# Optimization experiments

Measured on AMD Instinct MI355X. Metric: run time of the kernel, lower is better.

The kernel has to match this reference:

```python
import jax, jax.numpy as jnp
import numpy as np
import math

N_HEAD = 16
HEAD = 64
WINDOW = 256


def _split_heads(h, B, T):
    # [B,T,C] -> [B,H,T,hs]
    return h.reshape(B, T, N_HEAD, HEAD).transpose(0, 2, 1, 3)


def setup_inputs() -> dict:
    key = jax.random.key(0)
    ks = jax.random.split(key, 16)
    B, T, C = 4, 1024, 1024
    scale = 0.02
    inp = {}
    inp['x'] = jax.random.normal(ks[0], (B, T, C), jnp.float32)
    inp['pos_emb'] = jax.random.normal(ks[1], (B, T, C), jnp.float32)
    for i, n in enumerate(['Wq', 'Wk', 'Wv', 'Wpq', 'Wpk', 'Wo']):
        inp[n] = jax.random.normal(ks[2 + i], (C, C), jnp.float32) * scale
        inp['b' + n[1:]] = jnp.zeros((C,), jnp.float32)
    return inp


def reference(x, pos_emb, Wq, bq, Wk, bk, Wv, bv, Wpq, bpq, Wpk, bpk, Wo, bo):
    B, T, C = x.shape
    q = _split_heads(x @ Wq + bq, B, T)
    k = _split_heads(x @ Wk + bk, B, T)
    v = _split_heads(x @ Wv + bv, B, T)
    pq = _split_heads(pos_emb @ Wpq + bpq, B, T)
    pk = _split_heads(pos_emb @ Wpk + bpk, B, T)

    # content-content scores, pre-scaled by 1/sqrt(hs) as in the original
    wei = jnp.einsum('bhqd,bhkd->bhqk', q, k) * (HEAD ** -0.5)
    # disentangled content->position and position->content terms
    c2p = jnp.einsum('bhqd,bhkd->bhqk', q, pk)
    p2c = jnp.einsum('bhqd,bhkd->bhqk', pq, k)
    wei = (wei + c2p + p2c) * (1.0 / math.sqrt(3 * HEAD))

    # causal + local-window band mask: j <= i and j >= i - WINDOW
    i = jnp.arange(T)
    allowed = (i[None, :] <= i[:, None]) & (i[None, :] >= i[:, None] - WINDOW)
    wei = jnp.where(allowed[None, None], wei, -jnp.inf)

    # ALiBi bias on |i-j| with per-head slopes 2^(-(8/H)*(h+1))
    slopes = 2.0 ** (-(8.0 / N_HEAD) * jnp.arange(1, N_HEAD + 1, dtype=jnp.float32))
    dist = jnp.abs(i[None, :] - i[:, None]).astype(wei.dtype)
    wei = wei - slopes[None, :, None, None] * dist[None, None]

    wei = jax.nn.softmax(wei, axis=-1)  # masked entries -> 0
    out = jnp.einsum('bhqk,bhkd->bhqd', wei, v)
    out = out.transpose(0, 2, 1, 3).reshape(B, T, C)
    return out @ Wo + bo, wei
```

## Files before the change

### kernel.cpp

```cpp
#include <hip/hip_runtime.h>

#define NHEAD 16
#define WIN 256

typedef unsigned short u16;
typedef unsigned int u32;
typedef short bf16x8 __attribute__((ext_vector_type(8)));
typedef float floatx4 __attribute__((ext_vector_type(4)));
typedef u16 u16x4 __attribute__((ext_vector_type(4)));

__device__ __forceinline__ u16 f2bf(float f) {
    u32 u = __builtin_bit_cast(u32, f);
    u32 r = (u + 0x7fffu + ((u >> 16) & 1u)) >> 16;
    return (u16)r;
}
__device__ __forceinline__ float bf2f(u16 b) {
    u32 u = ((u32)b) << 16;
    return __builtin_bit_cast(float, u);
}

__device__ __forceinline__ void gload_lds16(const void* g, void* l) {
    __builtin_amdgcn_global_load_lds((const __attribute__((address_space(1))) u32*)g,
                                     (__attribute__((address_space(3))) u32*)l, 16, 0, 0);
}

__global__ void k_prep_in(const float* __restrict__ x, const float* __restrict__ pos,
                          u16* __restrict__ xb, u16* __restrict__ pb) {
    int i = blockIdx.x * 256 + threadIdx.x;
    const float* src = x; u16* dst = xb;
    int j = i;
    if (i >= 1048576) { src = pos; dst = pb; j = i - 1048576; }
    const floatx4 v = ((const floatx4*)src)[j];
    u16x4 o;
    o[0] = f2bf(v[0]); o[1] = f2bf(v[1]); o[2] = f2bf(v[2]); o[3] = f2bf(v[3]);
    ((u16x4*)dst)[j] = o;
}

__global__ void k_prep_w(const float* __restrict__ Wq, const float* __restrict__ Wk,
                         const float* __restrict__ Wv, const float* __restrict__ Wpq,
                         const float* __restrict__ Wpk, const float* __restrict__ Wo,
                         u16* __restrict__ wtqkv, u16* __restrict__ wtp, u16* __restrict__ wto) {
    __shared__ float tile[32][33];
    const int z = blockIdx.z;
    const float* W; u16* Wt;
    switch (z) {
        case 0: W = Wq;  Wt = wtqkv;           break;
        case 1: W = Wk;  Wt = wtqkv + 1048576; break;
        case 2: W = Wv;  Wt = wtqkv + 2097152; break;
        case 3: W = Wpq; Wt = wtp;             break;
        case 4: W = Wpk; Wt = wtp + 1048576;   break;
        default: W = Wo; Wt = wto;             break;
    }
    const int tx = threadIdx.x & 31, ty = threadIdx.x >> 5;
    const int nb = blockIdx.x << 5, kb = blockIdx.y << 5;
#pragma unroll
    for (int i = 0; i < 4; ++i)
        tile[ty + 8 * i][tx] = W[(size_t)(kb + ty + 8 * i) * 1024 + nb + tx];
    __syncthreads();
#pragma unroll
    for (int i = 0; i < 4; ++i)
        Wt[(size_t)(nb + ty + 8 * i) * 1024 + kb + tx] = f2bf(tile[tx][ty + 8 * i]);
}

__global__ void k_concat_bias(const float* __restrict__ bq, const float* __restrict__ bk,
                              const float* __restrict__ bv, const float* __restrict__ bpq,
                              const float* __restrict__ bpk,
                              float* __restrict__ bqkv, float* __restrict__ bp) {
    int i = blockIdx.x * 256 + threadIdx.x;
    if (i >= 5120) return;
    float v; float* d;
    if (i < 1024)      { v = bq[i];         d = bqkv + i; }
    else if (i < 2048) { v = bk[i - 1024];  d = bqkv + i; }
    else if (i < 3072) { v = bv[i - 2048];  d = bqkv + i; }
    else if (i < 4096) { v = bpq[i - 3072]; d = bp + (i - 3072); }
    else               { v = bpk[i - 4096]; d = bp + (i - 3072); }
    *d = v;
}

__launch_bounds__(256, 2)
__global__ void gemm_proj(const u16* __restrict__ A0, const u16* __restrict__ Bt0,
                          u16* __restrict__ C0, const float* __restrict__ bias0, int nblk0, int N0,
                          const u16* __restrict__ A1, const u16* __restrict__ Bt1,
                          u16* __restrict__ C1, const float* __restrict__ bias1, int N1,
                          int M, int K) {
    __shared__ u16 smA[128 * 64];
    __shared__ u16 smB[128 * 64];
    const int t = threadIdx.x;
    const int l = t & 63, w = t >> 6;
    const int bx = blockIdx.x;
    const u16* A; const u16* Bt; u16* C; const float* bias; int N, n0;
    if (bx < nblk0) { A = A0; Bt = Bt0; C = C0; bias = bias0; N = N0; n0 = bx << 7; }
    else            { A = A1; Bt = Bt1; C = C1; bias = bias1; N = N1; n0 = (bx - nblk0) << 7; }
    const int m0 = blockIdx.y << 7;
    const int wm = w & 1, wn = w >> 1;
    floatx4 acc[4][4];
#pragma unroll
    for (int a = 0; a < 4; ++a)
#pragma unroll
        for (int bq = 0; bq < 4; ++bq) { floatx4 z = {0.f, 0.f, 0.f, 0.f}; acc[a][bq] = z; }

    const int nkt = K >> 6;
    for (int kt = 0; kt < nkt; ++kt) {
        const int k0 = kt << 6;
#pragma unroll
        for (int i = 0; i < 4; ++i) {
            int o = (w << 12) + (i << 10) + (l << 4);
            int row = o >> 7, colb = o & 127;
            int sc = colb ^ ((row & 7) << 4);
            gload_lds16((const char*)A + ((size_t)(m0 + row) * K + k0) * 2 + sc,
                        (char*)smA + (w << 12) + (i << 10));
            gload_lds16((const char*)Bt + ((size_t)(n0 + row) * K + k0) * 2 + sc,
                        (char*)smB + (w << 12) + (i << 10));
        }
        __syncthreads();
#pragma unroll
        for (int ks = 0; ks < 2; ++ks) {
            const int kb = ((ks << 5) + ((l >> 4) << 3)) << 1;
            bf16x8 am[4], bn[4];
#pragma unroll
            for (int mt = 0; mt < 4; ++mt) {
                int row = (wm << 6) + (mt << 4) + (l & 15);
                am[mt] = *(const bf16x8*)((const char*)smA + row * 128 + (kb ^ ((row & 7) << 4)));
            }
#pragma unroll
            for (int nt = 0; nt < 4; ++nt) {
                int row = (wn << 6) + (nt << 4) + (l & 15);
                bn[nt] = *(const bf16x8*)((const char*)smB + row * 128 + (kb ^ ((row & 7) << 4)));
            }
#pragma unroll
            for (int mt = 0; mt < 4; ++mt)
#pragma unroll
                for (int nt = 0; nt < 4; ++nt)
                    acc[mt][nt] = __builtin_amdgcn_mfma_f32_16x16x32_bf16(am[mt], bn[nt], acc[mt][nt], 0, 0, 0);
        }
        __syncthreads();
    }
#pragma unroll
    for (int nt = 0; nt < 4; ++nt) {
        const int n = n0 + (wn << 6) + (nt << 4) + (l & 15);
        const float bv = bias[n];
#pragma unroll
        for (int mt = 0; mt < 4; ++mt) {
#pragma unroll
            for (int r = 0; r < 4; ++r) {
                int m = m0 + (wm << 6) + (mt << 4) + ((l >> 4) << 2) + r;
                C[(size_t)m * N + n] = f2bf(acc[mt][nt][r] + bv);
            }
        }
    }
}

__launch_bounds__(256, 2)
__global__ void gemm_bt_f32(const u16* __restrict__ A, const u16* __restrict__ Bt,
                            float* __restrict__ Cout, const float* __restrict__ bias,
                            int M, int N, int K) {
    __shared__ u16 smA[128 * 64];
    __shared__ u16 smB[128 * 64];
    const int t = threadIdx.x;
    const int l = t & 63, w = t >> 6;
    const int n0 = blockIdx.x << 7, m0 = blockIdx.y << 7;
    const int wm = w & 1, wn = w >> 1;
    floatx4 acc[4][4];
#pragma unroll
    for (int a = 0; a < 4; ++a)
#pragma unroll
        for (int bq = 0; bq < 4; ++bq) { floatx4 z = {0.f, 0.f, 0.f, 0.f}; acc[a][bq] = z; }

    const int nkt = K >> 6;
    for (int kt = 0; kt < nkt; ++kt) {
        const int k0 = kt << 6;
#pragma unroll
        for (int i = 0; i < 4; ++i) {
            int o = (w << 12) + (i << 10) + (l << 4);
            int row = o >> 7, colb = o & 127;
            int sc = colb ^ ((row & 7) << 4);
            gload_lds16((const char*)A + ((size_t)(m0 + row) * K + k0) * 2 + sc,
                        (char*)smA + (w << 12) + (i << 10));
            gload_lds16((const char*)Bt + ((size_t)(n0 + row) * K + k0) * 2 + sc,
                        (char*)smB + (w << 12) + (i << 10));
        }
        __syncthreads();
#pragma unroll
        for (int ks = 0; ks < 2; ++ks) {
            const int kb = ((ks << 5) + ((l >> 4) << 3)) << 1;
            bf16x8 am[4], bn[4];
#pragma unroll
            for (int mt = 0; mt < 4; ++mt) {
                int row = (wm << 6) + (mt << 4) + (l & 15);
                am[mt] = *(const bf16x8*)((const char*)smA + row * 128 + (kb ^ ((row & 7) << 4)));
            }
#pragma unroll
            for (int nt = 0; nt < 4; ++nt) {
                int row = (wn << 6) + (nt << 4) + (l & 15);
                bn[nt] = *(const bf16x8*)((const char*)smB + row * 128 + (kb ^ ((row & 7) << 4)));
            }
#pragma unroll
            for (int mt = 0; mt < 4; ++mt)
#pragma unroll
                for (int nt = 0; nt < 4; ++nt)
                    acc[mt][nt] = __builtin_amdgcn_mfma_f32_16x16x32_bf16(am[mt], bn[nt], acc[mt][nt], 0, 0, 0);
        }
        __syncthreads();
    }
#pragma unroll
    for (int nt = 0; nt < 4; ++nt) {
        const int n = n0 + (wn << 6) + (nt << 4) + (l & 15);
        const float bv = bias[n];
#pragma unroll
        for (int mt = 0; mt < 4; ++mt) {
#pragma unroll
            for (int r = 0; r < 4; ++r) {
                int m = m0 + (wm << 6) + (mt << 4) + ((l >> 4) << 2) + r;
                Cout[(size_t)m * N + n] = acc[mt][nt][r] + bv;
            }
        }
    }
}

__launch_bounds__(256, 2)
__global__ void k_attn(const u16* __restrict__ qkv, const u16* __restrict__ pqk,
                       float* __restrict__ wei, u16* __restrict__ att) {
    __shared__ __align__(16) char sm[50176];
    u16* smQ  = (u16*)(sm);
    u16* smPQ = (u16*)(sm + 8192);
    u16* smK  = (u16*)(sm + 16384);
    u16* smKm = (u16*)(sm + 24576);
    u16* smP  = (u16*)(sm);
    u16* smVt = (u16*)(sm + 41984);

    const int t = threadIdx.x, l = t & 63, w = t >> 6;
    const int qt = blockIdx.x, h = blockIdx.y, b = blockIdx.z;
    const int q0 = qt << 6;
    const int jlo = (q0 - WIN) > 0 ? (q0 - WIN) : 0;
    const int nch = (qt + 1) < 5 ? (qt + 1) : 5;
    const int col_l = l & 15;
    const int rq_hi = (l >> 4) << 2;

#pragma unroll
    for (int i = 0; i < 2; ++i) {
        int o = (w << 11) + (i << 10) + (l << 4);
        int row = o >> 7, colb = o & 127;
        int sc = colb ^ ((row & 7) << 4);
        gload_lds16((const char*)qkv + ((size_t)(b * 1024 + q0 + row) * 3072 + h * 64) * 2 + sc,
                    (char*)smQ + (w << 11) + (i << 10));
        gload_lds16((const char*)pqk + ((size_t)(b * 1024 + q0 + row) * 2048 + h * 64) * 2 + sc,
                    (char*)smPQ + (w << 11) + (i << 10));
    }

    {
        const int zlen1 = jlo;
        const int zstart2 = q0 + 64;
        const int nz4 = (zlen1 + (1024 - zstart2)) >> 2;
        float* wbase = wei + (((size_t)(b * NHEAD + h)) << 20);
        floatx4 z4 = {0.f, 0.f, 0.f, 0.f};
        for (int rr = w; rr < 64; rr += 4) {
            float* rowp = wbase + (((size_t)(q0 + rr)) << 10);
            for (int cc = l; cc < nz4; cc += 64) {
                int off4 = cc << 2;
                int col = (off4 < zlen1) ? off4 : (zstart2 + (off4 - zlen1));
                *(floatx4*)(rowp + col) = z4;
            }
        }
    }

    floatx4 acc[20];
#pragma unroll
    for (int i = 0; i < 20; ++i) { floatx4 z = {0.f, 0.f, 0.f, 0.f}; acc[i] = z; }

    const int prow = t >> 2, pd0 = (t & 3) << 4;
    bf16x8 rk0, rk1, rp0, rp1;
    {
        const u16* kp = qkv + (size_t)(b * 1024 + jlo + prow) * 3072 + 1024 + h * 64 + pd0;
        const u16* pp = pqk + (size_t)(b * 1024 + jlo + prow) * 2048 + 1024 + h * 64 + pd0;
        rk0 = *(const bf16x8*)kp; rk1 = *(const bf16x8*)(kp + 8);
        rp0 = *(const bf16x8*)pp; rp1 = *(const bf16x8*)(pp + 8);
    }
#pragma unroll
    for (int c = 0; c < 5; ++c) {
        if (c < nch) {
            const int jb = jlo + (c << 6);
            {
                bf16x8 o0, o1;
#pragma unroll
                for (int j = 0; j < 8; ++j) {
                    o0[j] = (short)f2bf(0.125f * bf2f((u16)rk0[j]) + bf2f((u16)rp0[j]));
                    o1[j] = (short)f2bf(0.125f * bf2f((u16)rk1[j]) + bf2f((u16)rp1[j]));
                }
                const int sw = (prow & 7) << 4;
                *(bf16x8*)((char*)smKm + prow * 128 + ((pd0 * 2) ^ sw)) = o0;
                *(bf16x8*)((char*)smKm + prow * 128 + ((pd0 * 2 + 16) ^ sw)) = o1;
            }
#pragma unroll
            for (int i = 0; i < 2; ++i) {
                int o = (w << 11) + (i << 10) + (l << 4);
                int row = o >> 7, colb = o & 127;
                int sc = colb ^ ((row & 7) << 4);
                gload_lds16((const char*)qkv + ((size_t)(b * 1024 + jb + row) * 3072 + 1024 + h * 64) * 2 + sc,
                            (char*)smK + (w << 11) + (i << 10));
            }
            __syncthreads();
            if (c + 1 < nch) {
                const int jb2 = jlo + ((c + 1) << 6);
                const u16* kp = qkv + (size_t)(b * 1024 + jb2 + prow) * 3072 + 1024 + h * 64 + pd0;
                const u16* pp = pqk + (size_t)(b * 1024 + jb2 + prow) * 2048 + 1024 + h * 64 + pd0;
                rk0 = *(const bf16x8*)kp; rk1 = *(const bf16x8*)(kp + 8);
                rp0 = *(const bf16x8*)pp; rp1 = *(const bf16x8*)(pp + 8);
            }
            __builtin_amdgcn_s_setprio(1);
#pragma unroll
            for (int ks = 0; ks < 2; ++ks) {
                const int kb = ((ks << 5) + ((l >> 4) << 3)) << 1;
                const int rq = (w << 4) + (l & 15);
                bf16x8 aQ  = *(const bf16x8*)((const char*)smQ  + rq * 128 + (kb ^ ((rq & 7) << 4)));
                bf16x8 aPQ = *(const bf16x8*)((const char*)smPQ + rq * 128 + (kb ^ ((rq & 7) << 4)));
#pragma unroll
                for (int s = 0; s < 4; ++s) {
                    const int rk = (s << 4) + (l & 15);
                    bf16x8 bKm = *(const bf16x8*)((const char*)smKm + rk * 128 + (kb ^ ((rk & 7) << 4)));
                    bf16x8 bK  = *(const bf16x8*)((const char*)smK  + rk * 128 + (kb ^ ((rk & 7) << 4)));
                    acc[c * 4 + s] = __builtin_amdgcn_mfma_f32_16x16x32_bf16(aQ,  bKm, acc[c * 4 + s], 0, 0, 0);
                    acc[c * 4 + s] = __builtin_amdgcn_mfma_f32_16x16x32_bf16(aPQ, bK,  acc[c * 4 + s], 0, 0, 0);
                }
            }
            __builtin_amdgcn_s_setprio(0);
            __syncthreads();
        }
    }

    const float inv_s192 = 0.07216878364870323f;
    const float slope = exp2f(-0.5f * (float)(h + 1));
    const int ntiles = nch << 2;
#pragma unroll
    for (int r = 0; r < 4; ++r) {
        const int iq = q0 + (w << 4) + rq_hi + r;
        float mx = -1e30f;
#pragma unroll
        for (int ti = 0; ti < 20; ++ti) {
            int j = jlo + (ti << 4) + col_l;
            float s = acc[ti][r] * inv_s192 - slope * (float)(iq - j);
            bool ok = (ti < ntiles) && (j <= iq) && (j >= iq - WIN);
            s = ok ? s : -1e30f;
            acc[ti][r] = s;
            mx = fmaxf(mx, s);
        }
        mx = fmaxf(mx, __shfl_xor(mx, 1));
        mx = fmaxf(mx, __shfl_xor(mx, 2));
        mx = fmaxf(mx, __shfl_xor(mx, 4));
        mx = fmaxf(mx, __shfl_xor(mx, 8));
        float sum = 0.f;
#pragma unroll
        for (int ti = 0; ti < 20; ++ti) {
            float p = __expf(acc[ti][r] - mx);
            acc[ti][r] = p;
            sum += p;
        }
        sum += __shfl_xor(sum, 1); sum += __shfl_xor(sum, 2);
        sum += __shfl_xor(sum, 4); sum += __shfl_xor(sum, 8);
        const float inv = 1.0f / sum;
        float* wrow = wei + ((((size_t)(b * NHEAD + h)) << 10) + iq) * 1024;
#pragma unroll
        for (int ti = 0; ti < 20; ++ti) {
            if (ti < ntiles) {
                float p = acc[ti][r] * inv;
                int j = jlo + (ti << 4) + col_l;
                wrow[j] = p;
                smP[((w << 4) + rq_hi + r) * 328 + (ti << 4) + col_l] = f2bf(p);
            }
        }
    }

    floatx4 acco[4];
#pragma unroll
    for (int s = 0; s < 4; ++s) { floatx4 z = {0.f, 0.f, 0.f, 0.f}; acco[s] = z; }
    const int vkey = t & 63, vdb = (t >> 6) << 4;
    bf16x8 v0, v1;
    {
        const u16* vp = qkv + (size_t)(b * 1024 + jlo + vkey) * 3072 + 2048 + h * 64 + vdb;
        v0 = *(const bf16x8*)vp; v1 = *(const bf16x8*)(vp + 8);
    }
#pragma unroll
    for (int c = 0; c < 5; ++c) {
        if (c < nch) {
            {
                const int kx = vkey << 1;
#pragma unroll
                for (int j = 0; j < 8; ++j) {
                    const int d0 = vdb + j, d1 = vdb + 8 + j;
                    *(u16*)((char*)smVt + d0 * 128 + (kx ^ ((d0 & 7) << 4))) = (u16)v0[j];
                    *(u16*)((char*)smVt + d1 * 128 + (kx ^ ((d1 & 7) << 4))) = (u16)v1[j];
                }
            }
            __syncthreads();
            if (c + 1 < nch) {
                const u16* vp = qkv + (size_t)(b * 1024 + jlo + ((c + 1) << 6) + vkey) * 3072 + 2048 + h * 64 + vdb;
                v0 = *(const bf16x8*)vp; v1 = *(const bf16x8*)(vp + 8);
            }
            __builtin_amdgcn_s_setprio(1);
#pragma unroll
            for (int ks = 0; ks < 2; ++ks) {
                const int rp = (w << 4) + (l & 15);
                const int keyb = ((c << 6) + (ks << 5) + ((l >> 4) << 3)) << 1;
                bf16x8 aP = *(const bf16x8*)((const char*)smP + rp * 656 + keyb);
                const int klb = ((ks << 5) + ((l >> 4) << 3)) << 1;
#pragma unroll
                for (int s = 0; s < 4; ++s) {
                    const int d = (s << 4) + col_l;
                    bf16x8 bV = *(const bf16x8*)((const char*)smVt + d * 128 + (klb ^ ((d & 7) << 4)));
                    acco[s] = __builtin_amdgcn_mfma_f32_16x16x32_bf16(aP, bV, acco[s], 0, 0, 0);
                }
            }
            __builtin_amdgcn_s_setprio(0);
            __syncthreads();
        }
    }
#pragma unroll
    for (int s = 0; s < 4; ++s) {
#pragma unroll
        for (int r = 0; r < 4; ++r) {
            const int iq = q0 + (w << 4) + rq_hi + r;
            const int d = (s << 4) + col_l;
            att[(((size_t)(b * 1024 + iq)) << 10) + h * 64 + d] = f2bf(acco[s][r]);
        }
    }
}

extern "C" void kernel_launch(void* const* d_in, const int* in_sizes, int n_in,
                              void* d_out, int out_size, void* d_ws, size_t ws_size,
                              hipStream_t stream) {
    const float* x   = (const float*)d_in[0];
    const float* pos = (const float*)d_in[1];
    const float* Wq  = (const float*)d_in[2];
    const float* bq  = (const float*)d_in[3];
    const float* Wk  = (const float*)d_in[4];
    const float* bk  = (const float*)d_in[5];
    const float* Wv  = (const float*)d_in[6];
    const float* bv  = (const float*)d_in[7];
    const float* Wpq = (const float*)d_in[8];
    const float* bpq = (const float*)d_in[9];
    const float* Wpk = (const float*)d_in[10];
    const float* bpk = (const float*)d_in[11];
    const float* Wo  = (const float*)d_in[12];
    const float* bo  = (const float*)d_in[13];

    char* ws = (char*)d_ws;
    u16*   xb    = (u16*)(ws);
    u16*   pb    = (u16*)(ws + 8388608);
    u16*   wtqkv = (u16*)(ws + 16777216);
    u16*   wtp   = (u16*)(ws + 23068672);
    u16*   wto   = (u16*)(ws + 27262976);
    float* bqkv  = (float*)(ws + 29360128);
    float* bp    = (float*)(ws + 29372416);
    u16*   qkv   = (u16*)(ws + 29380608);
    u16*   pqk   = (u16*)(ws + 54546432);
    u16*   att   = xb;

    float* out0 = (float*)d_out;
    float* wei  = (float*)d_out + 4194304;

    k_prep_in<<<8192, 256, 0, stream>>>(x, pos, xb, pb);
    k_prep_w<<<dim3(32, 32, 6), 256, 0, stream>>>(Wq, Wk, Wv, Wpq, Wpk, Wo, wtqkv, wtp, wto);
    k_concat_bias<<<20, 256, 0, stream>>>(bq, bk, bv, bpq, bpk, bqkv, bp);

    gemm_proj<<<dim3(40, 32), 256, 0, stream>>>(xb, wtqkv, qkv, bqkv, 24, 3072,
                                                pb, wtp, pqk, bp, 2048, 4096, 1024);

    k_attn<<<dim3(16, 16, 4), 256, 0, stream>>>(qkv, pqk, wei, att);

    gemm_bt_f32<<<dim3(8, 32), 256, 0, stream>>>(att, wto, out0, bo, 4096, 1024, 1024);
}
```

Baseline: 454.2 us.

## Merge prep kernels, shrink output GEMM N-tile, raise attention occupancy bound

The three preprocessing kernels (input conversion, weight transpose, bias concat) are folded into one launch that dispatches on block index, cutting launch overhead. The output projection GEMM now uses 128x64 tiles, doubling the grid from 256 to 512 blocks so the CUs are better filled. The attention kernel's launch bound goes from 2 to 3 waves per SIMD, which may force register spilling. The merged prep kernel also makes the elementwise blocks reserve shared memory they do not use.

```diff
diff --git a/kernel.cpp b/kernel.cpp
--- a/kernel.cpp
+++ b/kernel.cpp
@@ -24,57 +24,61 @@
                                      (__attribute__((address_space(3))) u32*)l, 16, 0, 0);
 }
 
-__global__ void k_prep_in(const float* __restrict__ x, const float* __restrict__ pos,
-                          u16* __restrict__ xb, u16* __restrict__ pb) {
-    int i = blockIdx.x * 256 + threadIdx.x;
-    const float* src = x; u16* dst = xb;
-    int j = i;
-    if (i >= 1048576) { src = pos; dst = pb; j = i - 1048576; }
-    const floatx4 v = ((const floatx4*)src)[j];
-    u16x4 o;
-    o[0] = f2bf(v[0]); o[1] = f2bf(v[1]); o[2] = f2bf(v[2]); o[3] = f2bf(v[3]);
-    ((u16x4*)dst)[j] = o;
-}
-
-__global__ void k_prep_w(const float* __restrict__ Wq, const float* __restrict__ Wk,
-                         const float* __restrict__ Wv, const float* __restrict__ Wpq,
-                         const float* __restrict__ Wpk, const float* __restrict__ Wo,
-                         u16* __restrict__ wtqkv, u16* __restrict__ wtp, u16* __restrict__ wto) {
+__global__ void k_prep(const float* __restrict__ x, const float* __restrict__ pos,
+                       u16* __restrict__ xb, u16* __restrict__ pb,
+                       const float* __restrict__ Wq, const float* __restrict__ Wk,
+                       const float* __restrict__ Wv, const float* __restrict__ Wpq,
+                       const float* __restrict__ Wpk, const float* __restrict__ Wo,
+                       u16* __restrict__ wtqkv, u16* __restrict__ wtp, u16* __restrict__ wto,
+                       const float* __restrict__ bq, const float* __restrict__ bk,
+                       const float* __restrict__ bv, const float* __restrict__ bpq,
+                       const float* __restrict__ bpk,
+                       float* __restrict__ bqkv, float* __restrict__ bp) {
     __shared__ float tile[32][33];
-    const int z = blockIdx.z;
-    const float* W; u16* Wt;
-    switch (z) {
-        case 0: W = Wq;  Wt = wtqkv;           break;
-        case 1: W = Wk;  Wt = wtqkv + 1048576; break;
-        case 2: W = Wv;  Wt = wtqkv + 2097152; break;
-        case 3: W = Wpq; Wt = wtp;             break;
-        case 4: W = Wpk; Wt = wtp + 1048576;   break;
-        default: W = Wo; Wt = wto;             break;
-    }
-    const int tx = threadIdx.x & 31, ty = threadIdx.x >> 5;
-    const int nb = blockIdx.x << 5, kb = blockIdx.y << 5;
-#pragma unroll
-    for (int i = 0; i < 4; ++i)
-        tile[ty + 8 * i][tx] = W[(size_t)(kb + ty + 8 * i) * 1024 + nb + tx];
-    __syncthreads();
-#pragma unroll
-    for (int i = 0; i < 4; ++i)
-        Wt[(size_t)(nb + ty + 8 * i) * 1024 + kb + tx] = f2bf(tile[tx][ty + 8 * i]);
-}
-
-__global__ void k_concat_bias(const float* __restrict__ bq, const float* __restrict__ bk,
-                              const float* __restrict__ bv, const float* __restrict__ bpq,
-                              const float* __restrict__ bpk,
-                              float* __restrict__ bqkv, float* __restrict__ bp) {
-    int i = blockIdx.x * 256 + threadIdx.x;
-    if (i >= 5120) return;
-    float v; float* d;
-    if (i < 1024)      { v = bq[i];         d = bqkv + i; }
-    else if (i < 2048) { v = bk[i - 1024];  d = bqkv + i; }
-    else if (i < 3072) { v = bv[i - 2048];  d = bqkv + i; }
-    else if (i < 4096) { v = bpq[i - 3072]; d = bp + (i - 3072); }
-    else               { v = bpk[i - 4096]; d = bp + (i - 3072); }
-    *d = v;
+    const int id = blockIdx.x;
+    if (id < 8192) {
+        int i = id * 256 + threadIdx.x;
+        const float* src = x; u16* dst = xb;
+        int j = i;
+        if (i >= 1048576) { src = pos; dst = pb; j = i - 1048576; }
+        const floatx4 v = ((const floatx4*)src)[j];
+        u16x4 o;
+        o[0] = f2bf(v[0]); o[1] = f2bf(v[1]); o[2] = f2bf(v[2]); o[3] = f2bf(v[3]);
+        ((u16x4*)dst)[j] = o;
+    } else if (id < 14336) {
+        const int wid = id - 8192;
+        const int z = wid >> 10, rem = wid & 1023;
+        const int bx = rem & 31, by = rem >> 5;
+        const float* W; u16* Wt;
+        switch (z) {
+            case 0: W = Wq;  Wt = wtqkv;           break;
+            case 1: W = Wk;  Wt = wtqkv + 1048576; break;
+            case 2: W = Wv;  Wt = wtqkv + 2097152; break;
+            case 3: W = Wpq; Wt = wtp;             break;
+            case 4: W = Wpk; Wt = wtp + 1048576;   break;
+            default: W = Wo; Wt = wto;             break;
+        }
+        const int tx = threadIdx.x & 31, ty = threadIdx.x >> 5;
+        const int nb = bx << 5, kb = by << 5;
+#pragma unroll
+        for (int i = 0; i < 4; ++i)
+            tile[ty + 8 * i][tx] = W[(size_t)(kb + ty + 8 * i) * 1024 + nb + tx];
+        __syncthreads();
+#pragma unroll
+        for (int i = 0; i < 4; ++i)
+            Wt[(size_t)(nb + ty + 8 * i) * 1024 + kb + tx] = f2bf(tile[tx][ty + 8 * i]);
+    } else {
+        int i = (id - 14336) * 256 + threadIdx.x;
+        if (i < 5120) {
+            float v; float* d;
+            if (i < 1024)      { v = bq[i];         d = bqkv + i; }
+            else if (i < 2048) { v = bk[i - 1024];  d = bqkv + i; }
+            else if (i < 3072) { v = bv[i - 2048];  d = bqkv + i; }
+            else if (i < 4096) { v = bpq[i - 3072]; d = bp + (i - 3072); }
+            else               { v = bpk[i - 4096]; d = bp + (i - 3072); }
+            *d = v;
+        }
+    }
 }
 
 __launch_bounds__(256, 2)
@@ -151,60 +155,66 @@
 }
 
 __launch_bounds__(256, 2)
-__global__ void gemm_bt_f32(const u16* __restrict__ A, const u16* __restrict__ Bt,
-                            float* __restrict__ Cout, const float* __restrict__ bias,
-                            int M, int N, int K) {
+__global__ void gemm_out(const u16* __restrict__ A, const u16* __restrict__ Bt,
+                         float* __restrict__ Cout, const float* __restrict__ bias,
+                         int M, int N, int K) {
     __shared__ u16 smA[128 * 64];
-    __shared__ u16 smB[128 * 64];
+    __shared__ u16 smB[64 * 64];
     const int t = threadIdx.x;
     const int l = t & 63, w = t >> 6;
-    const int n0 = blockIdx.x << 7, m0 = blockIdx.y << 7;
+    const int n0 = blockIdx.x << 6, m0 = blockIdx.y << 7;
     const int wm = w & 1, wn = w >> 1;
-    floatx4 acc[4][4];
+    floatx4 acc[4][2];
 #pragma unroll
     for (int a = 0; a < 4; ++a)
 #pragma unroll
-        for (int bq = 0; bq < 4; ++bq) { floatx4 z = {0.f, 0.f, 0.f, 0.f}; acc[a][bq] = z; }
+        for (int bq = 0; bq < 2; ++bq) { floatx4 z = {0.f, 0.f, 0.f, 0.f}; acc[a][bq] = z; }
 
     const int nkt = K >> 6;
     for (int kt = 0; kt < nkt; ++kt) {
         const int k0 = kt << 6;
 #pragma unroll
         for (int i = 0; i < 4; ++i) {
-            int o = (w << 12) + (i << 10) + (l << 4);
+            int o = (i << 12) + (t << 4);
             int row = o >> 7, colb = o & 127;
             int sc = colb ^ ((row & 7) << 4);
             gload_lds16((const char*)A + ((size_t)(m0 + row) * K + k0) * 2 + sc,
-                        (char*)smA + (w << 12) + (i << 10));
+                        (char*)smA + o);
+        }
+#pragma unroll
+        for (int i = 0; i < 2; ++i) {
+            int o = (i << 12) + (t << 4);
+            int row = o >> 7, colb = o & 127;
+            int sc = colb ^ ((row & 7) << 4);
             gload_lds16((const char*)Bt + ((size_t)(n0 + row) * K + k0) * 2 + sc,
-                        (char*)smB + (w << 12) + (i << 10));
+                        (char*)smB + o);
         }
         __syncthreads();
 #pragma unroll
         for (int ks = 0; ks < 2; ++ks) {
             const int kb = ((ks << 5) + ((l >> 4) << 3)) << 1;
-            bf16x8 am[4], bn[4];
+            bf16x8 am[4], bn[2];
 #pragma unroll
             for (int mt = 0; mt < 4; ++mt) {
                 int row = (wm << 6) + (mt << 4) + (l & 15);
                 am[mt] = *(const bf16x8*)((const char*)smA + row * 128 + (kb ^ ((row & 7) << 4)));
             }
 #pragma unroll
-            for (int nt = 0; nt < 4; ++nt) {
-                int row = (wn << 6) + (nt << 4) + (l & 15);
+            for (int nt = 0; nt < 2; ++nt) {
+                int row = (wn << 5) + (nt << 4) + (l & 15);
                 bn[nt] = *(const bf16x8*)((const char*)smB + row * 128 + (kb ^ ((row & 7) << 4)));
             }
 #pragma unroll
             for (int mt = 0; mt < 4; ++mt)
 #pragma unroll
-                for (int nt = 0; nt < 4; ++nt)
+                for (int nt = 0; nt < 2; ++nt)
                     acc[mt][nt] = __builtin_amdgcn_mfma_f32_16x16x32_bf16(am[mt], bn[nt], acc[mt][nt], 0, 0, 0);
         }
         __syncthreads();
     }
 #pragma unroll
-    for (int nt = 0; nt < 4; ++nt) {
-        const int n = n0 + (wn << 6) + (nt << 4) + (l & 15);
+    for (int nt = 0; nt < 2; ++nt) {
+        const int n = n0 + (wn << 5) + (nt << 4) + (l & 15);
         const float bv = bias[n];
 #pragma unroll
         for (int mt = 0; mt < 4; ++mt) {
@@ -217,7 +227,7 @@
     }
 }
 
-__launch_bounds__(256, 2)
+__launch_bounds__(256, 3)
 __global__ void k_attn(const u16* __restrict__ qkv, const u16* __restrict__ pqk,
                        float* __restrict__ wei, u16* __restrict__ att) {
     __shared__ __align__(16) char sm[50176];
@@ -457,14 +467,14 @@
     float* out0 = (float*)d_out;
     float* wei  = (float*)d_out + 4194304;
 
-    k_prep_in<<<8192, 256, 0, stream>>>(x, pos, xb, pb);
-    k_prep_w<<<dim3(32, 32, 6), 256, 0, stream>>>(Wq, Wk, Wv, Wpq, Wpk, Wo, wtqkv, wtp, wto);
-    k_concat_bias<<<20, 256, 0, stream>>>(bq, bk, bv, bpq, bpk, bqkv, bp);
+    k_prep<<<14356, 256, 0, stream>>>(x, pos, xb, pb,
+                                      Wq, Wk, Wv, Wpq, Wpk, Wo, wtqkv, wtp, wto,
+                                      bq, bk, bv, bpq, bpk, bqkv, bp);
 
     gemm_proj<<<dim3(40, 32), 256, 0, stream>>>(xb, wtqkv, qkv, bqkv, 24, 3072,
                                                 pb, wtp, pqk, bp, 2048, 4096, 1024);
 
     k_attn<<<dim3(16, 16, 4), 256, 0, stream>>>(qkv, pqk, wei, att);
 
-    gemm_bt_f32<<<dim3(8, 32), 256, 0, stream>>>(att, wto, out0, bo, 4096, 1024, 1024);
-}
+    gemm_out<<<dim3(16, 32), 256, 0, stream>>>(att, wto, out0, bo, 4096, 1024, 1024);
+}
```

Measured after the change: 446.7 us. About the same (-1.6%).
